# Optimization experiments

Measured on AMD Instinct MI355X. Metric: run time of the kernel, lower is better.

The kernel has to match this reference:

```python
import jax, jax.numpy as jnp
import numpy as np

LN_EPS = 1e-5

def layer_norm(x, w, b):
    m = jnp.mean(x, axis=-1, keepdims=True)
    v = jnp.mean((x - m) ** 2, axis=-1, keepdims=True)
    return (x - m) * jax.lax.rsqrt(v + LN_EPS) * w + b

def setup_inputs() -> dict:
    key = jax.random.key(0)
    ks = jax.random.split(key, 10)
    B, N, L = 32, 576, 100
    low, high = 1024, 1536
    inp = {
        "vit_feat": jax.random.normal(ks[0], (B, N, low), dtype=jnp.float32),
        "box_feat": jax.random.normal(ks[1], (B, L, high), dtype=jnp.float32),
        "lengths": jax.random.randint(ks[2], (B,), 0, L, dtype=jnp.int64),
        # query projector: LayerNorm(low) + Linear(low, low)
        "q_ln_w": jnp.ones((low,), jnp.float32),
        "q_ln_b": jnp.zeros((low,), jnp.float32),
        "q_w": jax.random.normal(ks[3], (low, low), dtype=jnp.float32) * 0.02,
        "q_b": jnp.zeros((low,), jnp.float32),
        # key projector: LayerNorm(high) + Linear(high, low)
        "k_ln_w": jnp.ones((high,), jnp.float32),
        "k_ln_b": jnp.zeros((high,), jnp.float32),
        "k_w": jax.random.normal(ks[4], (high, low), dtype=jnp.float32) * 0.02,
        "k_b": jnp.zeros((low,), jnp.float32),
        # value projector: LayerNorm(high) + Linear(high, low)
        "v_ln_w": jnp.ones((high,), jnp.float32),
        "v_ln_b": jnp.zeros((high,), jnp.float32),
        "v_w": jax.random.normal(ks[5], (high, low), dtype=jnp.float32) * 0.02,
        "v_b": jnp.zeros((low,), jnp.float32),
    }
    return inp

def reference(vit_feat, box_feat, lengths,
              q_ln_w, q_ln_b, q_w, q_b,
              k_ln_w, k_ln_b, k_w, k_b,
              v_ln_w, v_ln_b, v_w, v_b):
    B, L = box_feat.shape[0], box_feat.shape[1]
    # padding mask, same as the original per-row copy loop
    mask = jnp.arange(L)[None, :] < lengths[:, None]          # [B, L] bool
    q = layer_norm(vit_feat, q_ln_w, q_ln_b) @ q_w + q_b      # [B, N, low]
    k = layer_norm(box_feat, k_ln_w, k_ln_b) @ k_w + k_b      # [B, L, low]
    v = layer_norm(box_feat, v_ln_w, v_ln_b) @ v_w + v_b      # [B, L, low]
    scale = 1.0 / jnp.sqrt(jnp.asarray(k.shape[-1], q.dtype))
    att = jnp.einsum('bnd,bld->bnl', q, k * scale)            # [B, N, L]
    att = jnp.where(mask[:, None, :], att, -jnp.inf)
    att = jnp.nan_to_num(att)  # -inf -> finite min, matching torch nan_to_num
    att = jax.nn.softmax(att, axis=-1)
    out = jnp.einsum('bnl,bld->bnd', att, v)                  # [B, N, low]
    return vit_feat + out
```

## Files before the change

kernel.cpp:

```cpp
#include <hip/hip_runtime.h>
#include <stdint.h>

typedef __attribute__((ext_vector_type(8))) short short8;
typedef __attribute__((ext_vector_type(4))) float f32x4;

#define NEG_FLT_MAX (-3.402823466e38f)

__device__ __forceinline__ unsigned short f2bf(float f) {
  uint32_t u = __float_as_uint(f);
  uint32_t r = (u + 0x7fffu + ((u >> 16) & 1u)) >> 16;
  return (unsigned short)r;
}

__device__ __forceinline__ void gload16(const void* g, void* l) {
  __builtin_amdgcn_global_load_lds(
      (const __attribute__((address_space(1))) uint32_t*)g,
      (__attribute__((address_space(3))) uint32_t*)l, 16, 0, 0);
}

__global__ __launch_bounds__(256) void prep_kernel(
    const float* __restrict__ qw, const float* __restrict__ kw,
    const float* __restrict__ vw, const float* __restrict__ qb,
    const float* __restrict__ kb, float scale,
    unsigned short* __restrict__ qwb, unsigned short* __restrict__ kwb,
    unsigned short* __restrict__ vwt,
    float* __restrict__ bias3, float* __restrict__ w4, float* __restrict__ c4) {
  __shared__ float tile[32][33];
  const int bid = blockIdx.x;
  const int t = threadIdx.x;
  if (bid < 2560) {
    const int idx = bid * 256 + t;
    const int QG = 1024 * 1024 / 4;
    if (idx < QG) {
      float4 v = ((const float4*)qw)[idx];
      ushort4 o;
      o.x = f2bf(v.x); o.y = f2bf(v.y); o.z = f2bf(v.z); o.w = f2bf(v.w);
      ((ushort4*)qwb)[idx] = o;
    } else {
      const int j = idx - QG;
      float4 v = ((const float4*)kw)[j];
      ushort4 o;
      o.x = f2bf(v.x * scale); o.y = f2bf(v.y * scale);
      o.z = f2bf(v.z * scale); o.w = f2bf(v.w * scale);
      ((ushort4*)kwb)[j] = o;
    }
  } else if (bid < 4096) {
    const int j = bid - 2560;
    const int c0 = (j & 31) * 32, r0 = (j >> 5) * 32;
    const int tx = t & 31, ty = t >> 5;
#pragma unroll
    for (int i = ty; i < 32; i += 8)
      tile[i][tx] = vw[(size_t)(r0 + i) * 1024 + (c0 + tx)];
    __syncthreads();
#pragma unroll
    for (int i = ty; i < 32; i += 8)
      vwt[(size_t)(c0 + i) * 1536 + (r0 + tx)] = f2bf(tile[tx][i]);
  } else {
    const int idx = bid - 4096;
    const int wv = t >> 6, l = t & 63;
    float s = 0.f;
    if (idx < 256) {
      const int i = idx * 4 + wv;
      const float* row = qw + (size_t)i * 1024;
#pragma unroll
      for (int s0 = 0; s0 < 1024; s0 += 256) {
        float4 a = *(const float4*)(row + s0 + l * 4);
        float4 b = *(const float4*)(kb + s0 + l * 4);
        s += a.x * b.x + a.y * b.y + a.z * b.z + a.w * b.w;
      }
#pragma unroll
      for (int off = 32; off; off >>= 1) s += __shfl_xor(s, off);
      if (l == 0) bias3[i] = s * scale;
    } else if (idx < 640) {
      const int j = (idx - 256) * 4 + wv;
      const float* row = kw + (size_t)j * 1024;
#pragma unroll
      for (int s0 = 0; s0 < 1024; s0 += 256) {
        float4 a = *(const float4*)(row + s0 + l * 4);
        float4 b = *(const float4*)(qb + s0 + l * 4);
        s += a.x * b.x + a.y * b.y + a.z * b.z + a.w * b.w;
      }
#pragma unroll
      for (int off = 32; off; off >>= 1) s += __shfl_xor(s, off);
      if (l == 0) w4[j] = s * scale;
    } else if (wv == 0) {
#pragma unroll
      for (int s0 = 0; s0 < 1024; s0 += 256) {
        float4 a = *(const float4*)(qb + s0 + l * 4);
        float4 b = *(const float4*)(kb + s0 + l * 4);
        s += a.x * b.x + a.y * b.y + a.z * b.z + a.w * b.w;
      }
#pragma unroll
      for (int off = 32; off; off >>= 1) s += __shfl_xor(s, off);
      if (l == 0) *c4 = s * scale;
    }
  }
}

__device__ __forceinline__ void gemm_core64(
    const unsigned short* __restrict__ A, int lda, int rowmaxA, int tm0,
    const unsigned short* __restrict__ Bt, int ldb, int rowmaxB, int tn0,
    int K, unsigned short* As, unsigned short* Bs, f32x4 acc[4][4]) {
  const int tid = threadIdx.x;
  const int w = tid >> 6, l = tid & 63;
  const int wr = w >> 1, wc = w & 1;
  const int srow = (w << 4) + (l >> 2);
  const int scol = (l & 3) << 3;
  int ra0 = tm0 + srow;      if (ra0 > rowmaxA) ra0 = rowmaxA;
  int ra1 = tm0 + srow + 64; if (ra1 > rowmaxA) ra1 = rowmaxA;
  int rb0 = tn0 + srow;      if (rb0 > rowmaxB) rb0 = rowmaxB;
  int rb1 = tn0 + srow + 64; if (rb1 > rowmaxB) rb1 = rowmaxB;
  const unsigned short* pa0 = A + (size_t)ra0 * lda + scol;
  const unsigned short* pa1 = A + (size_t)ra1 * lda + scol;
  const unsigned short* pb0 = Bt + (size_t)rb0 * ldb + scol;
  const unsigned short* pb1 = Bt + (size_t)rb1 * ldb + scol;
  unsigned short* la0 = As + (w << 4) * 32;
  unsigned short* la1 = As + ((w << 4) + 64) * 32;
  unsigned short* lb0 = Bs + (w << 4) * 32;
  unsigned short* lb1 = Bs + ((w << 4) + 64) * 32;
  const int foff = ((l & 15) << 5) + ((l >> 4) << 3);
  const unsigned short* fa = As + (wr << 6) * 32 + foff;
  const unsigned short* fb = Bs + (wc << 6) * 32 + foff;
#pragma unroll
  for (int i = 0; i < 4; i++)
#pragma unroll
    for (int j = 0; j < 4; j++) acc[i][j] = (f32x4)0.0f;
  for (int k0 = 0; k0 < K; k0 += 64) {
    gload16(pa0 + k0, la0);
    gload16(pa1 + k0, la1);
    gload16(pb0 + k0, lb0);
    gload16(pb1 + k0, lb1);
    gload16(pa0 + k0 + 32, la0 + 4096);
    gload16(pa1 + k0 + 32, la1 + 4096);
    gload16(pb0 + k0 + 32, lb0 + 4096);
    gload16(pb1 + k0 + 32, lb1 + 4096);
    __syncthreads();
    {
      short8 a[4], b[4];
#pragma unroll
      for (int i = 0; i < 4; i++) a[i] = *(const short8*)(fa + i * 512);
#pragma unroll
      for (int j = 0; j < 4; j++) b[j] = *(const short8*)(fb + j * 512);
#pragma unroll
      for (int i = 0; i < 4; i++)
#pragma unroll
        for (int j = 0; j < 4; j++)
          acc[i][j] = __builtin_amdgcn_mfma_f32_16x16x32_bf16(a[i], b[j], acc[i][j], 0, 0, 0);
    }
    {
      short8 a[4], b[4];
#pragma unroll
      for (int i = 0; i < 4; i++) a[i] = *(const short8*)(fa + 4096 + i * 512);
#pragma unroll
      for (int j = 0; j < 4; j++) b[j] = *(const short8*)(fb + 4096 + j * 512);
#pragma unroll
      for (int i = 0; i < 4; i++)
#pragma unroll
        for (int j = 0; j < 4; j++)
          acc[i][j] = __builtin_amdgcn_mfma_f32_16x16x32_bf16(a[i], b[j], acc[i][j], 0, 0, 0);
    }
    __syncthreads();
  }
}

__global__ __launch_bounds__(256) void mid_kernel(
    const float* __restrict__ box,
    const float* __restrict__ klnw, const float* __restrict__ klnb,
    const float* __restrict__ vlnw, const float* __restrict__ vlnb,
    const unsigned short* __restrict__ qwb, const unsigned short* __restrict__ kwb,
    const float* __restrict__ w4v, const float* __restrict__ c4,
    unsigned short* __restrict__ kn, unsigned short* __restrict__ vn,
    unsigned short* __restrict__ W3, float* __restrict__ qbk) {
  __shared__ float red[8];
  __shared__ float redq[4];
  __shared__ unsigned short As[128 * 64];
  __shared__ unsigned short Bs[128 * 64];
  const int t = threadIdx.x;
  if (blockIdx.x < 3200) {
    const int row = blockIdx.x;
    const float4* xr = (const float4*)(box + (size_t)row * 1536);
    const float4 a = xr[t];
    float4 c = make_float4(0.f, 0.f, 0.f, 0.f);
    if (t < 128) c = xr[256 + t];
    float s = a.x + a.y + a.z + a.w + c.x + c.y + c.z + c.w;
    float ss = a.x * a.x + a.y * a.y + a.z * a.z + a.w * a.w +
               c.x * c.x + c.y * c.y + c.z * c.z + c.w * c.w;
#pragma unroll
    for (int off = 32; off > 0; off >>= 1) {
      s += __shfl_xor(s, off);
      ss += __shfl_xor(ss, off);
    }
    if ((t & 63) == 0) { red[(t >> 6) * 2] = s; red[(t >> 6) * 2 + 1] = ss; }
    __syncthreads();
    if (t == 0) {
      float aa = 0.f, bb = 0.f;
      for (int i = 0; i < 4; i++) { aa += red[i * 2]; bb += red[i * 2 + 1]; }
      red[0] = aa; red[1] = bb;
    }
    __syncthreads();
    s = red[0]; ss = red[1];
    const float m = s * (1.f / 1536.f);
    const float var = ss * (1.f / 1536.f) - m * m;
    const float rstd = rsqrtf(var + 1e-5f);
    float qd;
    {
      const float4 w4 = ((const float4*)klnw)[t];
      const float4 b4 = ((const float4*)klnb)[t];
      const float k0v = (a.x - m) * rstd * w4.x + b4.x;
      const float k1v = (a.y - m) * rstd * w4.y + b4.y;
      const float k2v = (a.z - m) * rstd * w4.z + b4.z;
      const float k3v = (a.w - m) * rstd * w4.w + b4.w;
      ushort4 o;
      o.x = f2bf(k0v); o.y = f2bf(k1v); o.z = f2bf(k2v); o.w = f2bf(k3v);
      ((ushort4*)(kn + (size_t)row * 1536))[t] = o;
      const float4 wq = ((const float4*)w4v)[t];
      qd = k0v * wq.x + k1v * wq.y + k2v * wq.z + k3v * wq.w;
      const float4 w4vv = ((const float4*)vlnw)[t];
      const float4 b4vv = ((const float4*)vlnb)[t];
      o.x = f2bf((a.x - m) * rstd * w4vv.x + b4vv.x);
      o.y = f2bf((a.y - m) * rstd * w4vv.y + b4vv.y);
      o.z = f2bf((a.z - m) * rstd * w4vv.z + b4vv.z);
      o.w = f2bf((a.w - m) * rstd * w4vv.w + b4vv.w);
      ((ushort4*)(vn + (size_t)row * 1536))[t] = o;
    }
    if (t < 128) {
      const int t2 = 256 + t;
      const float4 w4 = ((const float4*)klnw)[t2];
      const float4 b4 = ((const float4*)klnb)[t2];
      const float k0v = (c.x - m) * rstd * w4.x + b4.x;
      const float k1v = (c.y - m) * rstd * w4.y + b4.y;
      const float k2v = (c.z - m) * rstd * w4.z + b4.z;
      const float k3v = (c.w - m) * rstd * w4.w + b4.w;
      ushort4 o;
      o.x = f2bf(k0v); o.y = f2bf(k1v); o.z = f2bf(k2v); o.w = f2bf(k3v);
      ((ushort4*)(kn + (size_t)row * 1536))[t2] = o;
      const float4 wq = ((const float4*)w4v)[t2];
      qd += k0v * wq.x + k1v * wq.y + k2v * wq.z + k3v * wq.w;
      const float4 w4vv = ((const float4*)vlnw)[t2];
      const float4 b4vv = ((const float4*)vlnb)[t2];
      o.x = f2bf((c.x - m) * rstd * w4vv.x + b4vv.x);
      o.y = f2bf((c.y - m) * rstd * w4vv.y + b4vv.y);
      o.z = f2bf((c.z - m) * rstd * w4vv.z + b4vv.z);
      o.w = f2bf((c.w - m) * rstd * w4vv.w + b4vv.w);
      ((ushort4*)(vn + (size_t)row * 1536))[t2] = o;
    }
#pragma unroll
    for (int off = 32; off; off >>= 1) qd += __shfl_xor(qd, off);
    if ((t & 63) == 0) redq[t >> 6] = qd;
    __syncthreads();
    if (t == 0) qbk[row] = redq[0] + redq[1] + redq[2] + redq[3] + c4[0];
  } else {
    const int j = blockIdx.x - 3200;
    const int tm0 = (j & 7) * 128, tn0 = (j >> 3) * 128;
    f32x4 acc[4][4];
    gemm_core64(qwb, 1024, 1023, tm0, kwb, 1024, 1535, tn0, 1024, As, Bs, acc);
    const int w = t >> 6, l = t & 63;
    const int wr = w >> 1, wc = w & 1;
#pragma unroll
    for (int i = 0; i < 4; i++) {
      const int row0 = tm0 + wr * 64 + i * 16 + (l >> 4) * 4;
#pragma unroll
      for (int jj = 0; jj < 4; jj++) {
        const int col = tn0 + wc * 64 + jj * 16 + (l & 15);
#pragma unroll
        for (int r = 0; r < 4; r++)
          W3[(size_t)(row0 + r) * 1536 + col] = f2bf(acc[i][jj][r]);
      }
    }
  }
}

__global__ __launch_bounds__(256) void gemm_kv_kernel(
    const unsigned short* __restrict__ kn, const unsigned short* __restrict__ vn,
    const unsigned short* __restrict__ W3, const unsigned short* __restrict__ vwt,
    const float* __restrict__ bias3, const float* __restrict__ vb,
    unsigned short* __restrict__ kq, unsigned short* __restrict__ vT) {
  __shared__ unsigned short As[128 * 64];
  __shared__ unsigned short Bs[128 * 64];
  const int z = blockIdx.z;
  const unsigned short* A = z ? vn : kn;
  const unsigned short* Bt = z ? vwt : W3;
  const float* bias = z ? vb : bias3;
  const int M = 3200, N = 1024, K = 1536;
  const int tm0 = blockIdx.x * 128, tn0 = blockIdx.y * 128;
  f32x4 acc[4][4];
  gemm_core64(A, K, M - 1, tm0, Bt, K, N - 1, tn0, K, As, Bs, acc);
  const int tid = threadIdx.x;
  const int w = tid >> 6, l = tid & 63;
  const int wr = w >> 1, wc = w & 1;
#pragma unroll
  for (int i = 0; i < 4; i++) {
    const int row0 = tm0 + wr * 64 + i * 16 + (l >> 4) * 4;
#pragma unroll
    for (int j = 0; j < 4; j++) {
      const int col = tn0 + wc * 64 + j * 16 + (l & 15);
      const float bv = bias[col];
#pragma unroll
      for (int r = 0; r < 4; r++) {
        const int row = row0 + r;
        const float val = acc[i][j][r] + bv;
        if (!z) {
          kq[(size_t)row * N + col] = f2bf(val);
        } else {
          const int bb = row / 100;
          const int ll = row - bb * 100;
          vT[((size_t)bb * N + col) * 128 + ll] = f2bf(val);
        }
      }
    }
  }
}

__device__ __forceinline__ void block_reduce2(float& s, float& ss, float* red) {
#pragma unroll
  for (int off = 32; off > 0; off >>= 1) {
    s += __shfl_xor(s, off);
    ss += __shfl_xor(ss, off);
  }
  const int wave = threadIdx.x >> 6;
  const int lane = threadIdx.x & 63;
  if (lane == 0) { red[wave * 2] = s; red[wave * 2 + 1] = ss; }
  __syncthreads();
  if (threadIdx.x == 0) {
    float a = 0.f, b = 0.f;
    for (int i = 0; i < 4; i++) { a += red[i * 2]; b += red[i * 2 + 1]; }
    red[0] = a; red[1] = b;
  }
  __syncthreads();
  s = red[0]; ss = red[1];
}

__global__ __launch_bounds__(256) void ln_vit_kernel(
    const float* __restrict__ x, const float* __restrict__ w,
    const float* __restrict__ b, unsigned short* __restrict__ out) {
  __shared__ float red[8];
  const int row = blockIdx.x;
  const int t = threadIdx.x;
  const float4 v = ((const float4*)(x + (size_t)row * 1024))[t];
  float s = v.x + v.y + v.z + v.w;
  float ss = v.x * v.x + v.y * v.y + v.z * v.z + v.w * v.w;
  block_reduce2(s, ss, red);
  const float m = s * (1.f / 1024.f);
  const float var = ss * (1.f / 1024.f) - m * m;
  const float rstd = rsqrtf(var + 1e-5f);
  const float4 w4 = ((const float4*)w)[t];
  const float4 b4 = ((const float4*)b)[t];
  ushort4 o;
  o.x = f2bf((v.x - m) * rstd * w4.x + b4.x);
  o.y = f2bf((v.y - m) * rstd * w4.y + b4.y);
  o.z = f2bf((v.z - m) * rstd * w4.z + b4.z);
  o.w = f2bf((v.w - m) * rstd * w4.w + b4.w);
  ((ushort4*)(out + (size_t)row * 1024))[t] = o;
}

__global__ __launch_bounds__(256) void attfused_kernel(
    const unsigned short* __restrict__ qn, const unsigned short* __restrict__ kq,
    const unsigned short* __restrict__ vT, const float* __restrict__ qbk,
    const int* __restrict__ lengths, const float* __restrict__ vit,
    float* __restrict__ out) {
  __shared__ __align__(16) char smem[45824];
  float* Smat = (float*)smem;
  float* invr = (float*)(smem + 28672);
  float* qb_l = (float*)(smem + 28800);
  const int PB = 20480, BV = 29440;

  const int b = blockIdx.y;
  const int tm0 = blockIdx.x * 32;
  const int t = threadIdx.x;
  const int w = t >> 6, l = t & 63;
  const int lo = l & 15, hi = l >> 4;
  if (t < 128) qb_l[t] = (t < 100) ? qbk[b * 100 + t] : 0.f;

  const unsigned short* A = qn + (size_t)b * 576 * 1024;
  const unsigned short* B = kq + (size_t)b * 100 * 1024;
  const int ar = (t & 127) >> 2, ah = t >> 7, ac = (t & 3) << 3;
  const unsigned short* paA = A + (size_t)(tm0 + ar) * 1024 + ah * 32 + ac;
  const unsigned short* pbB[4];
#pragma unroll
  for (int i = 0; i < 4; i++) {
    int rb = (i & 1) * 64 + (t >> 2); if (rb > 99) rb = 99;
    pbB[i] = B + (size_t)rb * 1024 + (i >> 1) * 32 + ((t & 3) << 3);
  }
  const int cw = w << 5;

  f32x4 acc[2][2];
#pragma unroll
  for (int i = 0; i < 2; i++) { acc[i][0] = (f32x4)0.0f; acc[i][1] = (f32x4)0.0f; }

  for (int k0 = 0; k0 < 1024; k0 += 64) {
    gload16(paA + k0, smem + w * 1024);
#pragma unroll
    for (int i = 0; i < 4; i++)
      gload16(pbB[i] + k0, smem + 4096 + i * 4096 + w * 1024);
    __syncthreads();
#pragma unroll
    for (int half = 0; half < 2; half++) {
      short8 a[2], bb[2];
#pragma unroll
      for (int i = 0; i < 2; i++)
        a[i] = *(const short8*)(smem + half * 2048 + (i * 16 + lo) * 64 + hi * 16);
#pragma unroll
      for (int j = 0; j < 2; j++)
        bb[j] = *(const short8*)(smem + 4096 + half * 8192 + (cw + j * 16 + lo) * 64 + hi * 16);
#pragma unroll
      for (int i = 0; i < 2; i++)
#pragma unroll
        for (int j = 0; j < 2; j++)
          acc[i][j] = __builtin_amdgcn_mfma_f32_16x16x32_bf16(a[i], bb[j], acc[i][j], 0, 0, 0);
    }
    __syncthreads();
  }

#pragma unroll
  for (int i = 0; i < 2; i++) {
    const int r0 = i * 16 + hi * 4;
#pragma unroll
    for (int j = 0; j < 2; j++) {
      const int c = cw + j * 16 + lo;
      const float qb = qb_l[c];
#pragma unroll
      for (int rr = 0; rr < 4; rr++) Smat[c * 36 + r0 + rr] = acc[i][j][rr] + qb;
    }
  }
  __syncthreads();

  const int r = t >> 3, g = t & 7;
  const int len = lengths[b];
  float mx = NEG_FLT_MAX;
#pragma unroll
  for (int i = 0; i < 13; i++) {
    const int ll = g * 13 + i;
    if (ll < 100) {
      const float v = (ll < len) ? Smat[ll * 36 + r] : NEG_FLT_MAX;
      mx = fmaxf(mx, v);
    }
  }
  mx = fmaxf(mx, __shfl_xor(mx, 1));
  mx = fmaxf(mx, __shfl_xor(mx, 2));
  mx = fmaxf(mx, __shfl_xor(mx, 4));
  float sum = 0.f;
#pragma unroll
  for (int i = 0; i < 13; i++) {
    const int ll = g * 13 + i;
    if (ll < 100) {
      const float v = (ll < len) ? Smat[ll * 36 + r] : NEG_FLT_MAX;
      const float e = __expf(v - mx);
      Smat[ll * 36 + r] = e;
      sum += e;
    }
  }
  sum += __shfl_xor(sum, 1);
  sum += __shfl_xor(sum, 2);
  sum += __shfl_xor(sum, 4);
  if (g == 0) invr[r] = 1.f / sum;
  __syncthreads();

  {
    const float inv = invr[r];
#pragma unroll
    for (int jj = 0; jj < 4; jj++) {
      const int c0 = g * 16 + jj * 4;
      ushort4 o;
      o.x = (c0 + 0 < 100) ? f2bf(Smat[(c0 + 0) * 36 + r] * inv) : (unsigned short)0;
      o.y = (c0 + 1 < 100) ? f2bf(Smat[(c0 + 1) * 36 + r] * inv) : (unsigned short)0;
      o.z = (c0 + 2 < 100) ? f2bf(Smat[(c0 + 2) * 36 + r] * inv) : (unsigned short)0;
      o.w = (c0 + 3 < 100) ? f2bf(Smat[(c0 + 3) * 36 + r] * inv) : (unsigned short)0;
      const int phys = (r * 256 + g * 32 + jj * 8) ^ ((r & 7) << 4);
      *(ushort4*)(smem + PB + phys) = o;
    }
  }
  __syncthreads();

  const unsigned short* vTb = vT + (size_t)b * 131072;
  const float* vitb = vit + ((size_t)b * 576 + tm0) * 1024;
  float* outb = out + ((size_t)b * 576 + tm0) * 1024;
  const int sBcol = ((t & 15) ^ ((t >> 4) & 7)) << 3;
  for (int nt = 0; nt < 16; ++nt) {
#pragma unroll
    for (int i = 0; i < 4; i++) {
      const int vrow = nt * 64 + i * 16 + (t >> 4);
      gload16(vTb + (size_t)vrow * 128 + sBcol, smem + BV + i * 4096 + w * 1024);
    }
    __syncthreads();
    f32x4 acc2[2];
    acc2[0] = (f32x4)0.0f; acc2[1] = (f32x4)0.0f;
#pragma unroll
    for (int ks = 0; ks < 4; ks++) {
      short8 av[2], bv;
#pragma unroll
      for (int i = 0; i < 2; i++) {
        const int m = i * 16 + lo;
        av[i] = *(const short8*)(smem + PB + ((m * 256 + ks * 64 + hi * 16) ^ ((m & 7) << 4)));
      }
      const int n = (w << 4) + lo;
      bv = *(const short8*)(smem + BV + ((n * 256 + ks * 64 + hi * 16) ^ ((n & 7) << 4)));
      acc2[0] = __builtin_amdgcn_mfma_f32_16x16x32_bf16(av[0], bv, acc2[0], 0, 0, 0);
      acc2[1] = __builtin_amdgcn_mfma_f32_16x16x32_bf16(av[1], bv, acc2[1], 0, 0, 0);
    }
#pragma unroll
    for (int i = 0; i < 2; i++) {
      const int col = (w << 4) + lo;
#pragma unroll
      for (int rr = 0; rr < 4; rr++) {
        const int row = i * 16 + hi * 4 + rr;
        *(float*)(smem + ((row * 256 + col * 4) ^ ((row & 7) << 4))) = acc2[i][rr];
      }
    }
    __syncthreads();
#pragma unroll
    for (int m = 0; m < 2; m++) {
      const int row = m * 16 + (t >> 4);
      const int colb = (t & 15) * 4;
      float4 e = *(const float4*)(smem + ((row * 256 + colb * 4) ^ ((row & 7) << 4)));
      const size_t gidx = (size_t)row * 1024 + nt * 64 + colb;
      float4 vv = *(const float4*)(vitb + gidx);
      e.x += vv.x; e.y += vv.y; e.z += vv.z; e.w += vv.w;
      *(float4*)(outb + gidx) = e;
    }
    __syncthreads();
  }
}

extern "C" void kernel_launch(void* const* d_in, const int* in_sizes, int n_in,
                              void* d_out, int out_size, void* d_ws, size_t ws_size,
                              hipStream_t stream) {
  const float* vit = (const float*)d_in[0];
  const float* box = (const float*)d_in[1];
  const int* lengths = (const int*)d_in[2];
  const float* q_ln_w = (const float*)d_in[3];
  const float* q_ln_b = (const float*)d_in[4];
  const float* q_w = (const float*)d_in[5];
  const float* q_b = (const float*)d_in[6];
  const float* k_ln_w = (const float*)d_in[7];
  const float* k_ln_b = (const float*)d_in[8];
  const float* k_w = (const float*)d_in[9];
  const float* k_b = (const float*)d_in[10];
  const float* v_ln_w = (const float*)d_in[11];
  const float* v_ln_b = (const float*)d_in[12];
  const float* v_w = (const float*)d_in[13];
  const float* v_b = (const float*)d_in[14];
  float* out = (float*)d_out;
  char* ws = (char*)d_ws;

  unsigned short* kn    = (unsigned short*)(ws + 0);
  unsigned short* vn    = (unsigned short*)(ws + 9830400);
  unsigned short* v_wt  = (unsigned short*)(ws + 19660800);
  unsigned short* qwb   = (unsigned short*)(ws + 22806528);
  unsigned short* kwb   = (unsigned short*)(ws + 24903680);
  unsigned short* W3    = (unsigned short*)(ws + 28049408);
  float*          bias3 = (float*)(ws + 31195136);
  float*          w4    = (float*)(ws + 31199232);
  float*          c4    = (float*)(ws + 31207424);
  unsigned short* qn    = (unsigned short*)(ws + 0);
  float*          qbk   = (float*)(ws + 37748736);
  unsigned short* kq    = (unsigned short*)(ws + 37761536);
  unsigned short* vT    = (unsigned short*)(ws + 44315136);

  const float scale = 0.03125f;

  prep_kernel<<<4737, 256, 0, stream>>>(q_w, k_w, v_w, q_b, k_b, scale,
                                        qwb, kwb, v_wt, bias3, w4, c4);

  mid_kernel<<<3296, 256, 0, stream>>>(box, k_ln_w, k_ln_b, v_ln_w, v_ln_b,
                                       qwb, kwb, w4, c4, kn, vn, W3, qbk);

  gemm_kv_kernel<<<dim3(25, 8, 2), 256, 0, stream>>>(
      kn, vn, W3, v_wt, bias3, v_b, kq, vT);

  ln_vit_kernel<<<18432, 256, 0, stream>>>(vit, q_ln_w, q_ln_b, qn);

  attfused_kernel<<<dim3(18, 32), 256, 0, stream>>>(
      qn, kq, vT, qbk, lengths, vit, out);

  (void)in_sizes; (void)n_in; (void)out_size; (void)ws_size;
}
```

Baseline: 153.4 us.

## Merge KV GEMM with query LayerNorm launch and double-buffer attention epilogue

Combines the K/V projection GEMM and the vit LayerNorm into one launch: the first 400 blocks do GEMM tiles and the remaining blocks do LayerNorm rows. The qn buffer moves to a separate workspace region so it no longer aliases kn. This path is taken only when the workspace is large enough. In the attention kernel, the next V tile is prefetched while the epilogue runs, and the epilogue staging alternates between two shared-memory halves. The aim is to overlap the memory-bound LayerNorm with the compute-bound GEMM and hide V load latency. The cost is a larger shared-memory footprint per block in the merged kernel, which may lower occupancy for the LayerNorm blocks.

```diff
diff --git a/kernel.cpp b/kernel.cpp
--- a/kernel.cpp
+++ b/kernel.cpp
@@ -270,24 +270,14 @@
   }
 }
 
-__global__ __launch_bounds__(256) void gemm_kv_kernel(
-    const unsigned short* __restrict__ kn, const unsigned short* __restrict__ vn,
-    const unsigned short* __restrict__ W3, const unsigned short* __restrict__ vwt,
+__device__ __forceinline__ void kv_epilogue(
+    int z, int tm0, int tn0, f32x4 acc[4][4],
     const float* __restrict__ bias3, const float* __restrict__ vb,
     unsigned short* __restrict__ kq, unsigned short* __restrict__ vT) {
-  __shared__ unsigned short As[128 * 64];
-  __shared__ unsigned short Bs[128 * 64];
-  const int z = blockIdx.z;
-  const unsigned short* A = z ? vn : kn;
-  const unsigned short* Bt = z ? vwt : W3;
-  const float* bias = z ? vb : bias3;
-  const int M = 3200, N = 1024, K = 1536;
-  const int tm0 = blockIdx.x * 128, tn0 = blockIdx.y * 128;
-  f32x4 acc[4][4];
-  gemm_core64(A, K, M - 1, tm0, Bt, K, N - 1, tn0, K, As, Bs, acc);
   const int tid = threadIdx.x;
   const int w = tid >> 6, l = tid & 63;
   const int wr = w >> 1, wc = w & 1;
+  const float* bias = z ? vb : bias3;
 #pragma unroll
   for (int i = 0; i < 4; i++) {
     const int row0 = tm0 + wr * 64 + i * 16 + (l >> 4) * 4;
@@ -300,46 +290,38 @@
         const int row = row0 + r;
         const float val = acc[i][j][r] + bv;
         if (!z) {
-          kq[(size_t)row * N + col] = f2bf(val);
+          kq[(size_t)row * 1024 + col] = f2bf(val);
         } else {
           const int bb = row / 100;
           const int ll = row - bb * 100;
-          vT[((size_t)bb * N + col) * 128 + ll] = f2bf(val);
+          vT[((size_t)bb * 1024 + col) * 128 + ll] = f2bf(val);
         }
       }
     }
   }
 }
 
-__device__ __forceinline__ void block_reduce2(float& s, float& ss, float* red) {
-#pragma unroll
-  for (int off = 32; off > 0; off >>= 1) {
-    s += __shfl_xor(s, off);
-    ss += __shfl_xor(ss, off);
-  }
-  const int wave = threadIdx.x >> 6;
-  const int lane = threadIdx.x & 63;
-  if (lane == 0) { red[wave * 2] = s; red[wave * 2 + 1] = ss; }
-  __syncthreads();
-  if (threadIdx.x == 0) {
-    float a = 0.f, b = 0.f;
-    for (int i = 0; i < 4; i++) { a += red[i * 2]; b += red[i * 2 + 1]; }
-    red[0] = a; red[1] = b;
-  }
-  __syncthreads();
-  s = red[0]; ss = red[1];
-}
-
-__global__ __launch_bounds__(256) void ln_vit_kernel(
-    const float* __restrict__ x, const float* __restrict__ w,
-    const float* __restrict__ b, unsigned short* __restrict__ out) {
-  __shared__ float red[8];
-  const int row = blockIdx.x;
+__device__ __forceinline__ void ln_vit_row(
+    int row, const float* __restrict__ x, const float* __restrict__ w,
+    const float* __restrict__ b, unsigned short* __restrict__ out, float* red) {
   const int t = threadIdx.x;
   const float4 v = ((const float4*)(x + (size_t)row * 1024))[t];
   float s = v.x + v.y + v.z + v.w;
   float ss = v.x * v.x + v.y * v.y + v.z * v.z + v.w * v.w;
-  block_reduce2(s, ss, red);
+#pragma unroll
+  for (int off = 32; off > 0; off >>= 1) {
+    s += __shfl_xor(s, off);
+    ss += __shfl_xor(ss, off);
+  }
+  if ((t & 63) == 0) { red[(t >> 6) * 2] = s; red[(t >> 6) * 2 + 1] = ss; }
+  __syncthreads();
+  if (t == 0) {
+    float a = 0.f, bb = 0.f;
+    for (int i = 0; i < 4; i++) { a += red[i * 2]; bb += red[i * 2 + 1]; }
+    red[0] = a; red[1] = bb;
+  }
+  __syncthreads();
+  s = red[0]; ss = red[1];
   const float m = s * (1.f / 1024.f);
   const float var = ss * (1.f / 1024.f) - m * m;
   const float rstd = rsqrtf(var + 1e-5f);
@@ -353,6 +335,54 @@
   ((ushort4*)(out + (size_t)row * 1024))[t] = o;
 }
 
+__global__ __launch_bounds__(256) void gemm_kv_kernel(
+    const unsigned short* __restrict__ kn, const unsigned short* __restrict__ vn,
+    const unsigned short* __restrict__ W3, const unsigned short* __restrict__ vwt,
+    const float* __restrict__ bias3, const float* __restrict__ vb,
+    unsigned short* __restrict__ kq, unsigned short* __restrict__ vT) {
+  __shared__ unsigned short As[128 * 64];
+  __shared__ unsigned short Bs[128 * 64];
+  const int z = blockIdx.z;
+  const unsigned short* A = z ? vn : kn;
+  const unsigned short* Bt = z ? vwt : W3;
+  const int tm0 = blockIdx.x * 128, tn0 = blockIdx.y * 128;
+  f32x4 acc[4][4];
+  gemm_core64(A, 1536, 3199, tm0, Bt, 1536, 1023, tn0, 1536, As, Bs, acc);
+  kv_epilogue(z, tm0, tn0, acc, bias3, vb, kq, vT);
+}
+
+__global__ __launch_bounds__(256) void ln_vit_kernel(
+    const float* __restrict__ x, const float* __restrict__ w,
+    const float* __restrict__ b, unsigned short* __restrict__ out) {
+  __shared__ float red[8];
+  ln_vit_row(blockIdx.x, x, w, b, out, red);
+}
+
+__global__ __launch_bounds__(256) void kvln_kernel(
+    const unsigned short* __restrict__ kn, const unsigned short* __restrict__ vn,
+    const unsigned short* __restrict__ W3, const unsigned short* __restrict__ vwt,
+    const float* __restrict__ bias3, const float* __restrict__ vb,
+    unsigned short* __restrict__ kq, unsigned short* __restrict__ vT,
+    const float* __restrict__ vit, const float* __restrict__ qlnw,
+    const float* __restrict__ qlnb, unsigned short* __restrict__ qn) {
+  __shared__ float red[8];
+  __shared__ unsigned short As[128 * 64];
+  __shared__ unsigned short Bs[128 * 64];
+  const int bid = blockIdx.x;
+  if (bid < 400) {
+    const int z = bid / 200;
+    const int rem = bid - z * 200;
+    const int tm0 = (rem % 25) * 128, tn0 = (rem / 25) * 128;
+    const unsigned short* A = z ? vn : kn;
+    const unsigned short* Bt = z ? vwt : W3;
+    f32x4 acc[4][4];
+    gemm_core64(A, 1536, 3199, tm0, Bt, 1536, 1023, tn0, 1536, As, Bs, acc);
+    kv_epilogue(z, tm0, tn0, acc, bias3, vb, kq, vT);
+  } else {
+    ln_vit_row(bid - 400, vit, qlnw, qlnb, qn, red);
+  }
+}
+
 __global__ __launch_bounds__(256) void attfused_kernel(
     const unsigned short* __restrict__ qn, const unsigned short* __restrict__ kq,
     const unsigned short* __restrict__ vT, const float* __restrict__ qbk,
@@ -475,13 +505,18 @@
   const float* vitb = vit + ((size_t)b * 576 + tm0) * 1024;
   float* outb = out + ((size_t)b * 576 + tm0) * 1024;
   const int sBcol = ((t & 15) ^ ((t >> 4) & 7)) << 3;
+
+#define STAGE_D(nt) do {                                                      \
+    _Pragma("unroll")                                                         \
+    for (int i_ = 0; i_ < 4; i_++) {                                          \
+      const int vrow_ = (nt) * 64 + i_ * 16 + (t >> 4);                       \
+      gload16(vTb + (size_t)vrow_ * 128 + sBcol, smem + BV + i_ * 4096 + w * 1024); \
+    }                                                                         \
+  } while (0)
+
+  STAGE_D(0);
+  __syncthreads();
   for (int nt = 0; nt < 16; ++nt) {
-#pragma unroll
-    for (int i = 0; i < 4; i++) {
-      const int vrow = nt * 64 + i * 16 + (t >> 4);
-      gload16(vTb + (size_t)vrow * 128 + sBcol, smem + BV + i * 4096 + w * 1024);
-    }
-    __syncthreads();
     f32x4 acc2[2];
     acc2[0] = (f32x4)0.0f; acc2[1] = (f32x4)0.0f;
 #pragma unroll
@@ -497,21 +532,23 @@
       acc2[0] = __builtin_amdgcn_mfma_f32_16x16x32_bf16(av[0], bv, acc2[0], 0, 0, 0);
       acc2[1] = __builtin_amdgcn_mfma_f32_16x16x32_bf16(av[1], bv, acc2[1], 0, 0, 0);
     }
+    const int eb = (nt & 1) << 13;
 #pragma unroll
     for (int i = 0; i < 2; i++) {
       const int col = (w << 4) + lo;
 #pragma unroll
       for (int rr = 0; rr < 4; rr++) {
         const int row = i * 16 + hi * 4 + rr;
-        *(float*)(smem + ((row * 256 + col * 4) ^ ((row & 7) << 4))) = acc2[i][rr];
+        *(float*)(smem + eb + ((row * 256 + col * 4) ^ ((row & 7) << 4))) = acc2[i][rr];
       }
     }
     __syncthreads();
+    if (nt < 15) STAGE_D(nt + 1);
 #pragma unroll
     for (int m = 0; m < 2; m++) {
       const int row = m * 16 + (t >> 4);
       const int colb = (t & 15) * 4;
-      float4 e = *(const float4*)(smem + ((row * 256 + colb * 4) ^ ((row & 7) << 4)));
+      float4 e = *(const float4*)(smem + eb + ((row * 256 + colb * 4) ^ ((row & 7) << 4)));
       const size_t gidx = (size_t)row * 1024 + nt * 64 + colb;
       float4 vv = *(const float4*)(vitb + gidx);
       e.x += vv.x; e.y += vv.y; e.z += vv.z; e.w += vv.w;
@@ -519,6 +556,7 @@
     }
     __syncthreads();
   }
+#undef STAGE_D
 }
 
 extern "C" void kernel_launch(void* const* d_in, const int* in_sizes, int n_in,
@@ -551,10 +589,12 @@
   float*          bias3 = (float*)(ws + 31195136);
   float*          w4    = (float*)(ws + 31199232);
   float*          c4    = (float*)(ws + 31207424);
-  unsigned short* qn    = (unsigned short*)(ws + 0);
   float*          qbk   = (float*)(ws + 37748736);
   unsigned short* kq    = (unsigned short*)(ws + 37761536);
   unsigned short* vT    = (unsigned short*)(ws + 44315136);
+  const bool merged = (ws_size >= 90452480ull);
+  unsigned short* qn = merged ? (unsigned short*)(ws + 52703744)
+                              : (unsigned short*)(ws + 0);
 
   const float scale = 0.03125f;
 
@@ -564,10 +604,14 @@
   mid_kernel<<<3296, 256, 0, stream>>>(box, k_ln_w, k_ln_b, v_ln_w, v_ln_b,
                                        qwb, kwb, w4, c4, kn, vn, W3, qbk);
 
-  gemm_kv_kernel<<<dim3(25, 8, 2), 256, 0, stream>>>(
-      kn, vn, W3, v_wt, bias3, v_b, kq, vT);
-
-  ln_vit_kernel<<<18432, 256, 0, stream>>>(vit, q_ln_w, q_ln_b, qn);
+  if (merged) {
+    kvln_kernel<<<18832, 256, 0, stream>>>(kn, vn, W3, v_wt, bias3, v_b, kq, vT,
+                                           vit, q_ln_w, q_ln_b, qn);
+  } else {
+    gemm_kv_kernel<<<dim3(25, 8, 2), 256, 0, stream>>>(
+        kn, vn, W3, v_wt, bias3, v_b, kq, vT);
+    ln_vit_kernel<<<18432, 256, 0, stream>>>(vit, q_ln_w, q_ln_b, qn);
+  }
 
   attfused_kernel<<<dim3(18, 32), 256, 0, stream>>>(
       qn, kq, vT, qbk, lengths, vit, out);
```

New measurement: 172.1 us. 12.1% more time.
